# Performance work log

Hardware: AMD Instinct MI355X
Metric: run time of the kernel (lower is better)

## Reference

```python
import jax, jax.numpy as jnp
import numpy as np

N = 50000        # num_nodes
D = 512          # input_dim == output_dim (residual update requires equality)
EU = 100000      # undirected edges; directed E = 2*EU = 200000
STEP = 0.5       # step_size


def setup_inputs() -> dict:
    key = jax.random.key(0)
    ks = jax.random.split(key, 5)
    x = jax.random.normal(ks[0], (N, D), jnp.float32)
    # symmetric edge list without self loops: store (s,d) then (d,s)
    src = jax.random.randint(ks[1], (EU,), 0, N, dtype=jnp.int32)
    off = jax.random.randint(ks[2], (EU,), 1, N, dtype=jnp.int32)
    dst = (src + off) % N
    edge_index = jnp.stack([jnp.concatenate([src, dst]),
                            jnp.concatenate([dst, src])])  # [2, 2*EU]
    # reverse-edge index: edge e < EU reverses to e+EU and vice versa
    ar = jnp.arange(EU, dtype=jnp.int32)
    right_idx = jnp.concatenate([ar + EU, ar])
    # params: nn.Linear(D, D) and sheaf_learner nn.Linear(2D, 1, bias=False)
    W_lin = jax.random.normal(ks[3], (D, D), jnp.float32) / np.sqrt(D)
    b_lin = jnp.zeros((D,), jnp.float32)
    w_sheaf = jax.random.normal(ks[4], (2 * D,), jnp.float32) / np.sqrt(2 * D)
    return {"x": x, "W_lin": W_lin, "b_lin": b_lin, "w_sheaf": w_sheaf,
            "edge_index": edge_index, "right_idx": right_idx}


def reference(x, W_lin, b_lin, w_sheaf, edge_index, right_idx):
    row, col = edge_index[0], edge_index[1]
    d = x.shape[1]
    # sheaf_learner(cat([x_row, x_col])) == (x @ w[:d])[row] + (x @ w[d:])[col]
    s = x @ w_sheaf[:d]                      # [N]
    t = x @ w_sheaf[d:]                      # [N]
    maps = jnp.tanh(s[row] + t[col])         # [E] scalar restriction maps
    # off-diagonal Laplacian values: -F_e(row) * F_reverse(e)
    non_diag = -maps * maps[right_idx]       # [E]
    diag_maps = jax.ops.segment_sum(maps ** 2, row, num_segments=N)  # [N]
    d_inv = (diag_maps + 1.0) ** -0.5        # [N]
    norm_maps = d_inv[row] * non_diag * d_inv[col]                   # [E]
    diag = d_inv * diag_maps * d_inv                                 # [N]
    # y = linear(x); L @ y done as diag term + edge scatter
    y = x @ W_lin.T + b_lin                  # [N, D]
    Ly = diag[:, None] * y + jax.ops.segment_sum(
        norm_maps[:, None] * y[col], row, num_segments=N)
    return x - STEP * Ly
```

## Files before the change

### kernel.cpp

```cpp
#include <hip/hip_runtime.h>
#include <hip/hip_bf16.h>
#include <cstdint>
#include <cstddef>


#define DD 512
#define STEPSZ 0.5f
#define SLOTS 32

typedef __bf16 bf16;
typedef __bf16 bf16x8 __attribute__((ext_vector_type(8)));
typedef __bf16 bf16x4 __attribute__((ext_vector_type(4)));
typedef float f32x4 __attribute__((ext_vector_type(4)));

#define GLOAD16(g, l)                                                     \
  __builtin_amdgcn_global_load_lds(                                       \
      (const __attribute__((address_space(1))) void*)(g),                 \
      (__attribute__((address_space(3))) void*)(l), 16, 0, 0)
#define SB0() __builtin_amdgcn_sched_barrier(0)

__global__ __launch_bounds__(256) void k_prep(
    const float* __restrict__ x, const float* __restrict__ wsheaf,
    const float* __restrict__ wlin, bf16* __restrict__ xbf,
    bf16* __restrict__ wbf, float* __restrict__ s, float* __restrict__ t,
    float* __restrict__ dmaps, int* __restrict__ fill, int n) {
  if (blockIdx.x < 256) {
    int i = (blockIdx.x * 256 + threadIdx.x) * 4;
    float4 v = *(const float4*)(wlin + i);
    bf16x4 p;
    p[0] = (bf16)v.x; p[1] = (bf16)v.y; p[2] = (bf16)v.z; p[3] = (bf16)v.w;
    *(bf16x4*)(wbf + i) = p;
    int zi = blockIdx.x * 256 + threadIdx.x;
    if (zi < n) { dmaps[zi] = 0.0f; fill[zi] = 0; }
    return;
  }
  int lane = threadIdx.x & 63;
  int row = ((blockIdx.x - 256) << 2) + (threadIdx.x >> 6);
  if (row >= n) return;
  const float* xr = x + (size_t)row * DD + lane * 8;
  float4 a = *(const float4*)xr;
  float4 b = *(const float4*)(xr + 4);
  bf16x8 p;
  p[0] = (bf16)a.x; p[1] = (bf16)a.y; p[2] = (bf16)a.z; p[3] = (bf16)a.w;
  p[4] = (bf16)b.x; p[5] = (bf16)b.y; p[6] = (bf16)b.z; p[7] = (bf16)b.w;
  *(bf16x8*)(xbf + (size_t)row * DD + lane * 8) = p;
  const float* w1 = wsheaf + lane * 8;
  const float* w2 = wsheaf + DD + lane * 8;
  float4 wa = *(const float4*)w1, wb = *(const float4*)(w1 + 4);
  float4 wc = *(const float4*)w2, wd = *(const float4*)(w2 + 4);
  float sv = a.x * wa.x + a.y * wa.y + a.z * wa.z + a.w * wa.w +
             b.x * wb.x + b.y * wb.y + b.z * wb.z + b.w * wb.w;
  float tv = a.x * wc.x + a.y * wc.y + a.z * wc.z + a.w * wc.w +
             b.x * wd.x + b.y * wd.y + b.z * wd.z + b.w * wd.w;
  #pragma unroll
  for (int o = 32; o > 0; o >>= 1) {
    sv += __shfl_xor(sv, o);
    tv += __shfl_xor(tv, o);
  }
  if (lane == 0) { s[row] = sv; t[row] = tv; }
}

__global__ __launch_bounds__(256) void k_fill(
    const int* __restrict__ ei, const float* __restrict__ s,
    const float* __restrict__ t, float* __restrict__ dmaps,
    int* __restrict__ fill, int* __restrict__ ccol, float* __restrict__ cval,
    int E) {
  int e = blockIdx.x * 256 + threadIdx.x;
  if (e >= E) return;
  int r = ei[e], c = ei[E + e];
  float sr = s[r], tc = t[c], sc = s[c], tr = t[r];
  float me = tanhf(sr + tc);
  float mr = tanhf(sc + tr);
  atomicAdd(dmaps + r, me * me);
  int p = atomicAdd(fill + r, 1);
  if (p < SLOTS) {
    ccol[(size_t)r * SLOTS + p] = c;
    cval[(size_t)r * SLOTS + p] = -me * mr;
  }
}

__global__ __launch_bounds__(256) void k_gather(
    const bf16* __restrict__ xb, const float* __restrict__ dmaps,
    const int* __restrict__ fill, const int* __restrict__ ccol,
    const float* __restrict__ cval, bf16* __restrict__ u,
    float* __restrict__ cb, int n) {
  int lane = threadIdx.x & 63;
  int row = (blockIdx.x << 2) + (threadIdx.x >> 6);
  if (row >= n) return;
  int c0 = lane * 8;
  float dm = dmaps[row];
  float inv_r = rsqrtf(dm + 1.0f);
  float dg = dm / (dm + 1.0f);
  bf16x8 xv = *(const bf16x8*)(xb + (size_t)row * DD + c0);
  float acc[8];
  #pragma unroll
  for (int j = 0; j < 8; ++j) acc[j] = dg * (float)xv[j];
  int cnt = fill[row];
  if (cnt > SLOTS) cnt = SLOTS;
  const int* cc = ccol + (size_t)row * SLOTS;
  const float* cv = cval + (size_t)row * SLOTS;
  unsigned nm1 = (unsigned)(n - 1);
  float cbs = 0.0f;
  for (int i = 0; i < cnt; i += 4) {
    int4 c4 = *(const int4*)(cc + i);
    float4 v4 = *(const float4*)(cv + i);
    int rem = cnt - i;
    unsigned ca = min((unsigned)c4.x, nm1);
    unsigned cbi = min((unsigned)c4.y, nm1);
    unsigned cg = min((unsigned)c4.z, nm1);
    unsigned cd = min((unsigned)c4.w, nm1);
    bf16x8 na = *(const bf16x8*)(xb + (size_t)ca * DD + c0);
    bf16x8 nb = *(const bf16x8*)(xb + (size_t)cbi * DD + c0);
    bf16x8 ng = *(const bf16x8*)(xb + (size_t)cg * DD + c0);
    bf16x8 nd = *(const bf16x8*)(xb + (size_t)cd * DD + c0);
    float va = rem > 0 ? v4.x * inv_r * rsqrtf(dmaps[ca] + 1.0f) : 0.0f;
    float vb = rem > 1 ? v4.y * inv_r * rsqrtf(dmaps[cbi] + 1.0f) : 0.0f;
    float vg = rem > 2 ? v4.z * inv_r * rsqrtf(dmaps[cg] + 1.0f) : 0.0f;
    float vd = rem > 3 ? v4.w * inv_r * rsqrtf(dmaps[cd] + 1.0f) : 0.0f;
    cbs += va + vb + vg + vd;
    #pragma unroll
    for (int j = 0; j < 8; ++j)
      acc[j] += va * (float)na[j] + vb * (float)nb[j] + vg * (float)ng[j] +
                vd * (float)nd[j];
  }
  bf16x8 o;
  #pragma unroll
  for (int j = 0; j < 8; ++j) o[j] = (bf16)acc[j];
  *(bf16x8*)(u + (size_t)row * DD + c0) = o;
  if (lane == 0) cb[row] = dg + cbs;
}

__global__ __launch_bounds__(512, 4) void k_gemm(
    const bf16* __restrict__ ub, const bf16* __restrict__ wbf,
    const float* __restrict__ bias, const float* __restrict__ x,
    const bf16* __restrict__ xb, const float* __restrict__ cb,
    float* __restrict__ out, int M, int nwg, int use_bf) {
  __shared__ __align__(16) char smem[73728];
  bf16* lds = (bf16*)smem;
  int orig = blockIdx.x;
  int q = nwg >> 3, r = nwg & 7;
  int xcd = orig & 7;
  int wgid = (xcd < r ? xcd * (q + 1) : r * (q + 1) + (xcd - r) * q) +
             (orig >> 3);
  int bm = wgid >> 1, bn = wgid & 1;
  int tid = threadIdx.x, w = tid >> 6, lane = tid & 63;
  int wr = w >> 2, wc = w & 3;
  int lhi = lane >> 4;

  int row_local = lane >> 2;
  int kc = (lane & 3) ^ ((lane >> 3) & 3);
  int arloc = w * 16 + row_local;
  int gaR = bm * 128 + arloc;
  if (gaR > M - 1) gaR = M - 1;
  const bf16* gA = ub + (size_t)gaR * DD + kc * 8;
  bf16* lA = lds + (w * 16) * 32;
  const bf16* gB[2];
  bf16* lB[2];
  #pragma unroll
  for (int c = 0; c < 2; ++c) {
    int rloc = c * 128 + w * 16 + row_local;
    gB[c] = wbf + (size_t)(bn * 256 + rloc) * DD + kc * 8;
    lB[c] = lds + 4096 + (c * 128 + w * 16) * 32;
  }

  f32x4 acc[4][4] = {};
  int arow = (wr * 64 + (lane & 15)) * 32;
  int brow = (wc * 64 + (lane & 15)) * 32;
  int sl = (lhi ^ ((lane >> 1) & 3)) * 8;

  GLOAD16(gA, lA);
  GLOAD16(gB[0], lB[0]);
  GLOAD16(gB[1], lB[1]);
  GLOAD16(gA + 32, lA + 12288);
  GLOAD16(gB[0] + 32, lB[0] + 12288);
  GLOAD16(gB[1] + 32, lB[1] + 12288);

  #pragma unroll
  for (int t = 0; t < 16; ++t) {
    int cbuf = (t % 3) * 12288;
    if (t + 2 < 16) {
      int nbuf = ((t + 2) % 3) * 12288;
      int k0 = (t + 2) * 32;
      GLOAD16(gA + k0, lA + nbuf);
      GLOAD16(gB[0] + k0, lB[0] + nbuf);
      GLOAD16(gB[1] + k0, lB[1] + nbuf);
      asm volatile("s_waitcnt vmcnt(6)" ::: "memory");
    } else if (t + 1 < 16) {
      asm volatile("s_waitcnt vmcnt(3)" ::: "memory");
    } else {
      asm volatile("s_waitcnt vmcnt(0)" ::: "memory");
    }
    SB0();
    __builtin_amdgcn_s_barrier();
    SB0();
    const bf16* base = lds + cbuf;
    bf16x8 af[4], bfr[4];
    #pragma unroll
    for (int m = 0; m < 4; ++m)
      af[m] = *(const bf16x8*)(base + arow + m * 512 + sl);
    #pragma unroll
    for (int nn = 0; nn < 4; ++nn)
      bfr[nn] = *(const bf16x8*)(base + 4096 + brow + nn * 512 + sl);
    #pragma unroll
    for (int m = 0; m < 4; ++m)
      #pragma unroll
      for (int nn = 0; nn < 4; ++nn)
        acc[m][nn] = __builtin_amdgcn_mfma_f32_16x16x32_bf16(
            af[m], bfr[nn], acc[m][nn], 0, 0, 0);
    asm volatile("s_waitcnt lgkmcnt(0)" ::: "memory");
    SB0();
    __builtin_amdgcn_s_barrier();
    SB0();
  }

  int rowbase = bm * 128 + wr * 64;
  int clamped = rowbase + lane;
  if (clamped > M - 1) clamped = M - 1;
  float cbl = cb[clamped];
  float* ltile = (float*)smem + w * 2304;
  int prow = lane >> 3;
  int pc4 = lane & 7;
  #pragma unroll
  for (int h = 0; h < 2; ++h) {
    #pragma unroll
    for (int m = 0; m < 4; ++m)
      #pragma unroll
      for (int n2 = 0; n2 < 2; ++n2)
        #pragma unroll
        for (int rr = 0; rr < 4; ++rr) {
          int row = m * 16 + lhi * 4 + rr;
          ltile[row * 36 + n2 * 16 + (lane & 15)] = acc[m][h * 2 + n2][rr];
        }
    int gcol = bn * 256 + wc * 64 + h * 32 + pc4 * 4;
    float4 bb = *(const float4*)(bias + gcol);
    #pragma unroll
    for (int p = 0; p < 8; ++p) {
      int row = p * 8 + prow;
      int gr = rowbase + row;
      float cbr = __shfl(cbl, row);
      if (gr < M) {
        float4 v = *(const float4*)(ltile + row * 36 + pc4 * 4);
        float xr0, xr1, xr2, xr3;
        if (use_bf) {
          bf16x4 xv = *(const bf16x4*)(xb + (size_t)gr * DD + gcol);
          xr0 = (float)xv[0]; xr1 = (float)xv[1];
          xr2 = (float)xv[2]; xr3 = (float)xv[3];
        } else {
          float4 xv = *(const float4*)(x + (size_t)gr * DD + gcol);
          xr0 = xv.x; xr1 = xv.y; xr2 = xv.z; xr3 = xv.w;
        }
        float4 o;
        o.x = xr0 - STEPSZ * (v.x + cbr * bb.x);
        o.y = xr1 - STEPSZ * (v.y + cbr * bb.y);
        o.z = xr2 - STEPSZ * (v.z + cbr * bb.z);
        o.w = xr3 - STEPSZ * (v.w + cbr * bb.w);
        *(float4*)(out + (size_t)gr * DD + gcol) = o;
      }
    }
  }
}

extern "C" void kernel_launch(void* const* d_in, const int* in_sizes, int n_in,
                              void* d_out, int out_size, void* d_ws,
                              size_t ws_size, hipStream_t stream) {
  const float* x = (const float*)d_in[0];
  const float* W = (const float*)d_in[1];
  const float* b = (const float*)d_in[2];
  const float* wsheaf = (const float*)d_in[3];
  const int* ei = (const int*)d_in[4];
  const int* right = (const int*)d_in[5];
  (void)right;
  int N = in_sizes[0] / DD;
  int E = in_sizes[5];

  char* ws = (char*)d_ws;
  size_t p = 0;
  auto alloc = [&](size_t bytes) -> char* {
    char* r = ws + p;
    p += (bytes + 255) & ~(size_t)255;
    return r;
  };
  bf16* ub = (bf16*)alloc((size_t)N * DD * 2);
  float* cval = (float*)alloc((size_t)N * SLOTS * 4);
  int* ccol = (int*)alloc((size_t)N * SLOTS * 4);
  float* s = (float*)alloc((size_t)N * 4);
  float* t = (float*)alloc((size_t)N * 4);
  float* cb = (float*)alloc((size_t)N * 4);
  bf16* wbf = (bf16*)alloc((size_t)DD * DD * 2);
  char* zblock = alloc((size_t)N * 8);
  float* diag_maps = (float*)zblock;
  int* fill = (int*)(zblock + (size_t)N * 4);

  size_t xbf_bytes = (size_t)N * DD * 2;
  int use_bf = (p + xbf_bytes) <= ws_size;
  bf16* xbf = use_bf ? (bf16*)alloc(xbf_bytes) : (bf16*)d_out;

  k_prep<<<256 + (N + 3) / 4, 256, 0, stream>>>(x, wsheaf, W, xbf, wbf, s, t,
                                                diag_maps, fill, N);
  k_fill<<<(E + 255) / 256, 256, 0, stream>>>(ei, s, t, diag_maps, fill, ccol,
                                              cval, E);
  k_gather<<<(N + 3) / 4, 256, 0, stream>>>(xbf, diag_maps, fill, ccol, cval,
                                            ub, cb, N);
  int MT = (N + 127) / 128;
  int nwg = MT * 2;
  k_gemm<<<nwg, 512, 0, stream>>>(ub, wbf, b, x, xbf, cb, (float*)d_out, N,
                                  nwg, use_bf);
}
```

Before: 159.1 us.

## Split edge fill to pre-normalize edge weights and gather two rows per wave

The edge fill is split into two kernels. The first accumulates degree sums; the second folds the symmetric degree normalization into each stored edge value, so the gather no longer does random dmaps lookups and rsqrt per neighbor. The gather kernel now processes two rows per wavefront, keeping eight neighbor loads in flight per iteration to raise memory-level parallelism. The cost is an extra launch and a second pass over the edge list and s/t, plus more registers per thread in the gather.

```diff
diff --git a/kernel.cpp b/kernel.cpp
--- a/kernel.cpp
+++ b/kernel.cpp
@@ -60,9 +60,19 @@
   if (lane == 0) { s[row] = sv; t[row] = tv; }
 }
 
-__global__ __launch_bounds__(256) void k_fill(
+__global__ __launch_bounds__(256) void k_fill1(
     const int* __restrict__ ei, const float* __restrict__ s,
-    const float* __restrict__ t, float* __restrict__ dmaps,
+    const float* __restrict__ t, float* __restrict__ dmaps, int E) {
+  int e = blockIdx.x * 256 + threadIdx.x;
+  if (e >= E) return;
+  int r = ei[e], c = ei[E + e];
+  float me = tanhf(s[r] + t[c]);
+  atomicAdd(dmaps + r, me * me);
+}
+
+__global__ __launch_bounds__(256) void k_fill2(
+    const int* __restrict__ ei, const float* __restrict__ s,
+    const float* __restrict__ t, const float* __restrict__ dmaps,
     int* __restrict__ fill, int* __restrict__ ccol, float* __restrict__ cval,
     int E) {
   int e = blockIdx.x * 256 + threadIdx.x;
@@ -71,11 +81,11 @@
   float sr = s[r], tc = t[c], sc = s[c], tr = t[r];
   float me = tanhf(sr + tc);
   float mr = tanhf(sc + tr);
-  atomicAdd(dmaps + r, me * me);
+  float nm = -me * mr * rsqrtf((dmaps[r] + 1.0f) * (dmaps[c] + 1.0f));
   int p = atomicAdd(fill + r, 1);
   if (p < SLOTS) {
     ccol[(size_t)r * SLOTS + p] = c;
-    cval[(size_t)r * SLOTS + p] = -me * mr;
+    cval[(size_t)r * SLOTS + p] = nm;
   }
 }
 
@@ -85,49 +95,78 @@
     const float* __restrict__ cval, bf16* __restrict__ u,
     float* __restrict__ cb, int n) {
   int lane = threadIdx.x & 63;
-  int row = (blockIdx.x << 2) + (threadIdx.x >> 6);
-  if (row >= n) return;
+  int wv = threadIdx.x >> 6;
+  int rA = blockIdx.x * 8 + wv * 2;
+  if (rA >= n) return;
+  int rB = rA + 1;
+  int hasB = (rB < n);
+  int rBe = hasB ? rB : rA;
   int c0 = lane * 8;
-  float dm = dmaps[row];
-  float inv_r = rsqrtf(dm + 1.0f);
-  float dg = dm / (dm + 1.0f);
-  bf16x8 xv = *(const bf16x8*)(xb + (size_t)row * DD + c0);
-  float acc[8];
-  #pragma unroll
-  for (int j = 0; j < 8; ++j) acc[j] = dg * (float)xv[j];
-  int cnt = fill[row];
-  if (cnt > SLOTS) cnt = SLOTS;
-  const int* cc = ccol + (size_t)row * SLOTS;
-  const float* cv = cval + (size_t)row * SLOTS;
   unsigned nm1 = (unsigned)(n - 1);
-  float cbs = 0.0f;
-  for (int i = 0; i < cnt; i += 4) {
-    int4 c4 = *(const int4*)(cc + i);
-    float4 v4 = *(const float4*)(cv + i);
-    int rem = cnt - i;
-    unsigned ca = min((unsigned)c4.x, nm1);
-    unsigned cbi = min((unsigned)c4.y, nm1);
-    unsigned cg = min((unsigned)c4.z, nm1);
-    unsigned cd = min((unsigned)c4.w, nm1);
-    bf16x8 na = *(const bf16x8*)(xb + (size_t)ca * DD + c0);
-    bf16x8 nb = *(const bf16x8*)(xb + (size_t)cbi * DD + c0);
-    bf16x8 ng = *(const bf16x8*)(xb + (size_t)cg * DD + c0);
-    bf16x8 nd = *(const bf16x8*)(xb + (size_t)cd * DD + c0);
-    float va = rem > 0 ? v4.x * inv_r * rsqrtf(dmaps[ca] + 1.0f) : 0.0f;
-    float vb = rem > 1 ? v4.y * inv_r * rsqrtf(dmaps[cbi] + 1.0f) : 0.0f;
-    float vg = rem > 2 ? v4.z * inv_r * rsqrtf(dmaps[cg] + 1.0f) : 0.0f;
-    float vd = rem > 3 ? v4.w * inv_r * rsqrtf(dmaps[cd] + 1.0f) : 0.0f;
-    cbs += va + vb + vg + vd;
-    #pragma unroll
-    for (int j = 0; j < 8; ++j)
-      acc[j] += va * (float)na[j] + vb * (float)nb[j] + vg * (float)ng[j] +
-                vd * (float)nd[j];
-  }
-  bf16x8 o;
-  #pragma unroll
-  for (int j = 0; j < 8; ++j) o[j] = (bf16)acc[j];
-  *(bf16x8*)(u + (size_t)row * DD + c0) = o;
-  if (lane == 0) cb[row] = dg + cbs;
+
+  float dmA = dmaps[rA], dmB = dmaps[rBe];
+  float dgA = dmA / (dmA + 1.0f);
+  float dgB = dmB / (dmB + 1.0f);
+  bf16x8 xvA = *(const bf16x8*)(xb + (size_t)rA * DD + c0);
+  bf16x8 xvB = *(const bf16x8*)(xb + (size_t)rBe * DD + c0);
+  float accA[8], accB[8];
+  #pragma unroll
+  for (int j = 0; j < 8; ++j) {
+    accA[j] = dgA * (float)xvA[j];
+    accB[j] = dgB * (float)xvB[j];
+  }
+  int cntA = min(fill[rA], SLOTS);
+  int cntB = hasB ? min(fill[rBe], SLOTS) : 0;
+  const int* ccA = ccol + (size_t)rA * SLOTS;
+  const float* cvA = cval + (size_t)rA * SLOTS;
+  const int* ccB = ccol + (size_t)rBe * SLOTS;
+  const float* cvB = cval + (size_t)rBe * SLOTS;
+  float cbsA = 0.0f, cbsB = 0.0f;
+  int mx = max(cntA, cntB);
+  for (int i = 0; i < mx; i += 4) {
+    int4 cA = *(const int4*)(ccA + i);
+    float4 vA = *(const float4*)(cvA + i);
+    int4 cB = *(const int4*)(ccB + i);
+    float4 vB = *(const float4*)(cvB + i);
+    int remA = cntA - i, remB = cntB - i;
+    unsigned a0 = min((unsigned)cA.x, nm1), a1 = min((unsigned)cA.y, nm1);
+    unsigned a2 = min((unsigned)cA.z, nm1), a3 = min((unsigned)cA.w, nm1);
+    unsigned b0 = min((unsigned)cB.x, nm1), b1 = min((unsigned)cB.y, nm1);
+    unsigned b2 = min((unsigned)cB.z, nm1), b3 = min((unsigned)cB.w, nm1);
+    bf16x8 nA0 = *(const bf16x8*)(xb + (size_t)a0 * DD + c0);
+    bf16x8 nA1 = *(const bf16x8*)(xb + (size_t)a1 * DD + c0);
+    bf16x8 nA2 = *(const bf16x8*)(xb + (size_t)a2 * DD + c0);
+    bf16x8 nA3 = *(const bf16x8*)(xb + (size_t)a3 * DD + c0);
+    bf16x8 nB0 = *(const bf16x8*)(xb + (size_t)b0 * DD + c0);
+    bf16x8 nB1 = *(const bf16x8*)(xb + (size_t)b1 * DD + c0);
+    bf16x8 nB2 = *(const bf16x8*)(xb + (size_t)b2 * DD + c0);
+    bf16x8 nB3 = *(const bf16x8*)(xb + (size_t)b3 * DD + c0);
+    float wA0 = remA > 0 ? vA.x : 0.0f, wA1 = remA > 1 ? vA.y : 0.0f;
+    float wA2 = remA > 2 ? vA.z : 0.0f, wA3 = remA > 3 ? vA.w : 0.0f;
+    float wB0 = remB > 0 ? vB.x : 0.0f, wB1 = remB > 1 ? vB.y : 0.0f;
+    float wB2 = remB > 2 ? vB.z : 0.0f, wB3 = remB > 3 ? vB.w : 0.0f;
+    cbsA += wA0 + wA1 + wA2 + wA3;
+    cbsB += wB0 + wB1 + wB2 + wB3;
+    #pragma unroll
+    for (int j = 0; j < 8; ++j) {
+      accA[j] += wA0 * (float)nA0[j] + wA1 * (float)nA1[j] +
+                 wA2 * (float)nA2[j] + wA3 * (float)nA3[j];
+      accB[j] += wB0 * (float)nB0[j] + wB1 * (float)nB1[j] +
+                 wB2 * (float)nB2[j] + wB3 * (float)nB3[j];
+    }
+  }
+  bf16x8 oA, oB;
+  #pragma unroll
+  for (int j = 0; j < 8; ++j) {
+    oA[j] = (bf16)accA[j];
+    oB[j] = (bf16)accB[j];
+  }
+  *(bf16x8*)(u + (size_t)rA * DD + c0) = oA;
+  if (lane == 0) cb[rA] = dgA + cbsA;
+  if (hasB) {
+    *(bf16x8*)(u + (size_t)rB * DD + c0) = oB;
+    if (lane == 0) cb[rB] = dgB + cbsB;
+  }
 }
 
 __global__ __launch_bounds__(512, 4) void k_gemm(
@@ -297,9 +336,10 @@
 
   k_prep<<<256 + (N + 3) / 4, 256, 0, stream>>>(x, wsheaf, W, xbf, wbf, s, t,
                                                 diag_maps, fill, N);
-  k_fill<<<(E + 255) / 256, 256, 0, stream>>>(ei, s, t, diag_maps, fill, ccol,
-                                              cval, E);
-  k_gather<<<(N + 3) / 4, 256, 0, stream>>>(xbf, diag_maps, fill, ccol, cval,
+  k_fill1<<<(E + 255) / 256, 256, 0, stream>>>(ei, s, t, diag_maps, E);
+  k_fill2<<<(E + 255) / 256, 256, 0, stream>>>(ei, s, t, diag_maps, fill,
+                                               ccol, cval, E);
+  k_gather<<<(N + 7) / 8, 256, 0, stream>>>(xbf, diag_maps, fill, ccol, cval,
                                             ub, cb, N);
   int MT = (N + 127) / 128;
   int nwg = MT * 2;
```

Result: slower. 163.3 us (+2.6%).
